# Performance work log

Measured on AMD Instinct MI355X. Metric: run time of the kernel, lower is better.

The kernel has to match this reference:

```python
import jax, jax.numpy as jnp
import numpy as np

K = 5  # AUTKC top-K parameter


def setup_inputs() -> dict:
    key = jax.random.key(0)
    k1, k2 = jax.random.split(key)
    B, C = 4096, 32000
    pred = jax.random.normal(k1, (B, C), dtype=jnp.float32)
    y = jax.random.randint(k2, (B,), 0, C, dtype=jnp.int64)
    return {"pred": pred, "y": y, "epoch": 1}


def reference(pred, y, epoch):
    # epoch >= epoch_to_paced (=0), so the main AUTKC branch runs.
    B, C = pred.shape
    # surrogate != 'Hinge' -> softmax over classes
    probs = jax.nn.softmax(pred, axis=-1)                      # [B, C]
    pred_p = probs[jnp.arange(B), y][:, None]                  # [B, 1] positive-class prob
    pos_mask = jnp.arange(C)[None, :] == y[:, None]            # [B, C] boolean one-hot
    # Mask out the positive entry; top_k(K+1) over negatives == sort desc + take K+1.
    neg = jnp.where(pos_mask, -jnp.inf, probs)                 # [B, C]
    top_n, _ = jax.lax.top_k(neg, K + 1)                       # [B, K+1]
    # 'Sq' surrogate: (1 + s_neg - s_pos)^2
    loss = jnp.sum((1.0 + top_n - pred_p) ** 2, axis=-1) / K   # [B]
    return jnp.mean(loss)
```

## Files before the change

kernel.cpp:

```cpp
#include <hip/hip_runtime.h>
#include <math.h>

#define BLOCK 256
#define KTOP 6
#define KDIV 5.0f

__global__ __launch_bounds__(BLOCK)
void autkc_row_kernel(const float* __restrict__ pred,
                      const int* __restrict__ y,
                      float* __restrict__ row_loss,
                      int C) {
    const int row = blockIdx.x;
    const int tid = threadIdx.x;
    const float4* p4 = (const float4*)(pred + (size_t)row * (size_t)C);
    const int yy = y[row];

    const float NEG = -INFINITY;
    float t[KTOP];
#pragma unroll
    for (int k = 0; k < KTOP; ++k) t[k] = NEG;
    float s = 0.0f;
    float py = NEG;

    const int nvec = C >> 2;
    for (int i = tid; i < nvec; i += BLOCK) {
        float4 v = p4[i];
        const int base = i << 2;
        float vals[4] = {v.x, v.y, v.z, v.w};
#pragma unroll
        for (int c = 0; c < 4; ++c) {
            float vv = vals[c];
            s += __expf(vv);
            const int idx = base + c;
            if (idx == yy) { py = vv; vv = NEG; }
            if (vv > t[KTOP - 1]) {
                float nt[KTOP];
                nt[0] = fmaxf(t[0], vv);
#pragma unroll
                for (int k = 1; k < KTOP; ++k)
                    nt[k] = fmaxf(t[k], fminf(t[k - 1], vv));
#pragma unroll
                for (int k = 0; k < KTOP; ++k) t[k] = nt[k];
            }
        }
    }

    __shared__ float red[BLOCK][9];
#pragma unroll
    for (int k = 0; k < KTOP; ++k) red[tid][k] = t[k];
    red[tid][6] = s;
    red[tid][7] = py;
    __syncthreads();

    for (int half = BLOCK / 2; half >= 1; half >>= 1) {
        if (tid < half) {
            float a[KTOP], b[KTOP];
#pragma unroll
            for (int k = 0; k < KTOP; ++k) {
                a[k] = red[tid][k];
                b[k] = red[tid + half][k];
            }
            float c[KTOP];
#pragma unroll
            for (int k = 0; k < KTOP; ++k) {
                float best = NEG;
#pragma unroll
                for (int i = 0; i <= k + 1; ++i) {
                    const int bi = (k - i) >= 0 ? (k - i) : 0;
                    float av = (i > 0) ? a[i - 1] : INFINITY;
                    float bv = ((k + 1 - i) > 0) ? b[bi] : INFINITY;
                    best = fmaxf(best, fminf(av, bv));
                }
                c[k] = best;
            }
#pragma unroll
            for (int k = 0; k < KTOP; ++k) red[tid][k] = c[k];
            red[tid][6] = red[tid][6] + red[tid + half][6];
            red[tid][7] = fmaxf(red[tid][7], red[tid + half][7]);
        }
        __syncthreads();
    }

    if (tid == 0) {
        const float S   = red[0][6];
        const float inv = 1.0f / S;
        const float pp  = __expf(red[0][7]) * inv;
        float acc = 0.0f;
#pragma unroll
        for (int k = 0; k < KTOP; ++k) {
            const float pn = __expf(red[0][k]) * inv;
            const float d  = 1.0f + pn - pp;
            acc += d * d;
        }
        row_loss[row] = acc * (1.0f / KDIV);
    }
}

__global__ __launch_bounds__(BLOCK)
void autkc_reduce_kernel(const float* __restrict__ row_loss,
                         float* __restrict__ out, int B) {
    __shared__ float sh[BLOCK];
    const int tid = threadIdx.x;
    float s = 0.0f;
    for (int i = tid; i < B; i += BLOCK) s += row_loss[i];
    sh[tid] = s;
    __syncthreads();
    for (int half = BLOCK / 2; half >= 1; half >>= 1) {
        if (tid < half) sh[tid] += sh[tid + half];
        __syncthreads();
    }
    if (tid == 0) out[0] = sh[0] / (float)B;
}

extern "C" void kernel_launch(void* const* d_in, const int* in_sizes, int n_in,
                              void* d_out, int out_size, void* d_ws, size_t ws_size,
                              hipStream_t stream) {
    const float* pred = (const float*)d_in[0];
    const int*   y    = (const int*)d_in[1];

    const int B = in_sizes[1];
    const int C = in_sizes[0] / B;

    float* row_loss = (float*)d_ws;

    autkc_row_kernel<<<B, BLOCK, 0, stream>>>(pred, y, row_loss, C);
    autkc_reduce_kernel<<<1, BLOCK, 0, stream>>>(row_loss, (float*)d_out, B);
}
```

Before: 117.6 us.

## Track top-7 with branchless med3 insertion and drop positive-class masking from hot loop

The hot loop no longer compares each index against the label. It keeps a branch-free top-7 list using the fmed3 instruction, and afterwards removes the positive-class value from that list to get the top-6 negatives. The positive logit is read directly from global memory. Loads are unrolled four ways with four separate exp accumulators to raise memory-level parallelism. The final reduce uses 1024 threads and float4 loads. The trade-offs are one more top-k slot in every thread's insertion and merge work, and ties with the positive value are removed by value equality rather than by index.

```diff
diff --git a/kernel.cpp b/kernel.cpp
--- a/kernel.cpp
+++ b/kernel.cpp
@@ -2,8 +2,21 @@
 #include <math.h>
 
 #define BLOCK 256
-#define KTOP 6
-#define KDIV 5.0f
+#define KTOP 7
+#define RBLK 1024
+
+__device__ __forceinline__ void proc4(const float4 v, float& s, float t[KTOP]) {
+    float vals[4] = {v.x, v.y, v.z, v.w};
+#pragma unroll
+    for (int c = 0; c < 4; ++c) {
+        const float x = vals[c];
+        s += __expf(x);
+#pragma unroll
+        for (int k = KTOP - 1; k >= 1; --k)
+            t[k] = __builtin_amdgcn_fmed3f(t[k - 1], t[k], x);
+        t[0] = fmaxf(t[0], x);
+    }
+}
 
 __global__ __launch_bounds__(BLOCK)
 void autkc_row_kernel(const float* __restrict__ pred,
@@ -12,44 +25,36 @@
                       int C) {
     const int row = blockIdx.x;
     const int tid = threadIdx.x;
-    const float4* p4 = (const float4*)(pred + (size_t)row * (size_t)C);
+    const float* prow = pred + (size_t)row * (size_t)C;
+    const float4* p4 = (const float4*)prow;
+    const int nvec = C >> 2;
+
     const int yy = y[row];
+    const float py = prow[yy];
 
-    const float NEG = -INFINITY;
     float t[KTOP];
 #pragma unroll
-    for (int k = 0; k < KTOP; ++k) t[k] = NEG;
-    float s = 0.0f;
-    float py = NEG;
+    for (int k = 0; k < KTOP; ++k) t[k] = -INFINITY;
+    float s0 = 0.f, s1 = 0.f, s2 = 0.f, s3 = 0.f;
 
-    const int nvec = C >> 2;
-    for (int i = tid; i < nvec; i += BLOCK) {
-        float4 v = p4[i];
-        const int base = i << 2;
-        float vals[4] = {v.x, v.y, v.z, v.w};
-#pragma unroll
-        for (int c = 0; c < 4; ++c) {
-            float vv = vals[c];
-            s += __expf(vv);
-            const int idx = base + c;
-            if (idx == yy) { py = vv; vv = NEG; }
-            if (vv > t[KTOP - 1]) {
-                float nt[KTOP];
-                nt[0] = fmaxf(t[0], vv);
-#pragma unroll
-                for (int k = 1; k < KTOP; ++k)
-                    nt[k] = fmaxf(t[k], fminf(t[k - 1], vv));
-#pragma unroll
-                for (int k = 0; k < KTOP; ++k) t[k] = nt[k];
-            }
-        }
+    int i = tid;
+    for (; i + 3 * BLOCK < nvec; i += 4 * BLOCK) {
+        float4 a = p4[i];
+        float4 b = p4[i + BLOCK];
+        float4 c = p4[i + 2 * BLOCK];
+        float4 d = p4[i + 3 * BLOCK];
+        proc4(a, s0, t);
+        proc4(b, s1, t);
+        proc4(c, s2, t);
+        proc4(d, s3, t);
     }
+    for (; i < nvec; i += BLOCK) proc4(p4[i], s0, t);
+    const float s = (s0 + s1) + (s2 + s3);
 
     __shared__ float red[BLOCK][9];
 #pragma unroll
     for (int k = 0; k < KTOP; ++k) red[tid][k] = t[k];
-    red[tid][6] = s;
-    red[tid][7] = py;
+    red[tid][KTOP] = s;
     __syncthreads();
 
     for (int half = BLOCK / 2; half >= 1; half >>= 1) {
@@ -63,49 +68,63 @@
             float c[KTOP];
 #pragma unroll
             for (int k = 0; k < KTOP; ++k) {
-                float best = NEG;
+                float best = -INFINITY;
 #pragma unroll
-                for (int i = 0; i <= k + 1; ++i) {
-                    const int bi = (k - i) >= 0 ? (k - i) : 0;
-                    float av = (i > 0) ? a[i - 1] : INFINITY;
-                    float bv = ((k + 1 - i) > 0) ? b[bi] : INFINITY;
+                for (int m = 0; m <= k + 1; ++m) {
+                    const int bi = (k - m) >= 0 ? (k - m) : 0;
+                    float av = (m > 0) ? a[m - 1] : INFINITY;
+                    float bv = ((k + 1 - m) > 0) ? b[bi] : INFINITY;
                     best = fmaxf(best, fminf(av, bv));
                 }
                 c[k] = best;
             }
 #pragma unroll
             for (int k = 0; k < KTOP; ++k) red[tid][k] = c[k];
-            red[tid][6] = red[tid][6] + red[tid + half][6];
-            red[tid][7] = fmaxf(red[tid][7], red[tid + half][7]);
+            red[tid][KTOP] = red[tid][KTOP] + red[tid + half][KTOP];
         }
         __syncthreads();
     }
 
     if (tid == 0) {
-        const float S   = red[0][6];
+        float m[KTOP];
+#pragma unroll
+        for (int k = 0; k < KTOP; ++k) m[k] = red[0][k];
+        const float S   = red[0][KTOP];
         const float inv = 1.0f / S;
-        const float pp  = __expf(red[0][7]) * inv;
+        const float pp  = __expf(py) * inv;
+
+        int r = KTOP;
+#pragma unroll
+        for (int k = KTOP - 1; k >= 0; --k)
+            if (m[k] == py) r = k;
+
         float acc = 0.0f;
 #pragma unroll
-        for (int k = 0; k < KTOP; ++k) {
-            const float pn = __expf(red[0][k]) * inv;
-            const float d  = 1.0f + pn - pp;
+        for (int j = 0; j < 6; ++j) {
+            const float nv = (j < r) ? m[j] : m[j + 1];
+            const float d  = 1.0f + __expf(nv) * inv - pp;
             acc += d * d;
         }
-        row_loss[row] = acc * (1.0f / KDIV);
+        row_loss[row] = acc * 0.2f;
     }
 }
 
-__global__ __launch_bounds__(BLOCK)
+__global__ __launch_bounds__(RBLK)
 void autkc_reduce_kernel(const float* __restrict__ row_loss,
                          float* __restrict__ out, int B) {
-    __shared__ float sh[BLOCK];
+    __shared__ float sh[RBLK];
     const int tid = threadIdx.x;
     float s = 0.0f;
-    for (int i = tid; i < B; i += BLOCK) s += row_loss[i];
+    const int n4 = B >> 2;
+    const float4* r4 = (const float4*)row_loss;
+    for (int i = tid; i < n4; i += RBLK) {
+        float4 v = r4[i];
+        s += (v.x + v.y) + (v.z + v.w);
+    }
+    for (int i = (n4 << 2) + tid; i < B; i += RBLK) s += row_loss[i];
     sh[tid] = s;
     __syncthreads();
-    for (int half = BLOCK / 2; half >= 1; half >>= 1) {
+    for (int half = RBLK / 2; half >= 1; half >>= 1) {
         if (tid < half) sh[tid] += sh[tid + half];
         __syncthreads();
     }
@@ -124,5 +143,5 @@
     float* row_loss = (float*)d_ws;
 
     autkc_row_kernel<<<B, BLOCK, 0, stream>>>(pred, y, row_loss, C);
-    autkc_reduce_kernel<<<1, BLOCK, 0, stream>>>(row_loss, (float*)d_out, B);
+    autkc_reduce_kernel<<<1, RBLK, 0, stream>>>(row_loss, (float*)d_out, B);
 }
```

After: 101.1 us. -14.0%, faster.
